# Kernel optimization log

Measured on AMD Instinct MI355X. Metric: run time of the kernel, lower is better.

Reference implementation:

```python
import jax, jax.numpy as jnp
import numpy as np

N_NODES = 50000
N_EDGES = 800000
IN_CH = 128
HID = 128


def setup_inputs() -> dict:
    key = jax.random.key(0)
    ks = jax.random.split(key, 16)
    inp = {
        "x": jax.random.normal(ks[0], (N_NODES, IN_CH), dtype=jnp.float32),
        "edge_index": jax.random.randint(ks[1], (2, N_EDGES), 0, N_NODES, dtype=jnp.int64),
        "batch_size": 1024,
    }
    dims = [(IN_CH, HID), (HID, HID), (HID, HID)]
    for i, (din, dout) in enumerate(dims):
        s = 1.0 / np.sqrt(din)
        inp[f"W_l{i}"] = jax.random.uniform(ks[2 + 4 * i], (dout, din), jnp.float32, -s, s)
        inp[f"b_l{i}"] = jax.random.uniform(ks[3 + 4 * i], (dout,), jnp.float32, -s, s)
        inp[f"W_r{i}"] = jax.random.uniform(ks[4 + 4 * i], (dout, din), jnp.float32, -s, s)
        inp[f"a{i}"] = jnp.full((dout,), 0.25, dtype=jnp.float32)  # PReLU slope
    return inp


def _sage_prelu(x, src, dst, W_l, b_l, W_r, a):
    # mean aggregation of source messages at target nodes
    msg_sum = jax.ops.segment_sum(x[src], dst, num_segments=N_NODES)  # [N, din]
    deg = jax.ops.segment_sum(jnp.ones((src.shape[0],), x.dtype), dst, num_segments=N_NODES)
    agg = msg_sum / jnp.maximum(deg, 1.0)[:, None]
    out = agg @ W_l.T + b_l + x @ W_r.T  # lin_l(aggr) + lin_r(x), bias on lin_l only
    return jnp.where(out > 0, out, a * out)  # per-channel PReLU


def reference(x, edge_index, batch_size, W_l0, b_l0, W_r0, a0, W_l1, b_l1, W_r1, a1, W_l2, b_l2, W_r2, a2):
    src, dst = edge_index[0], edge_index[1]
    x = _sage_prelu(x, src, dst, W_l0, b_l0, W_r0, a0)
    x = _sage_prelu(x, src, dst, W_l1, b_l1, W_r1, a1)
    x = _sage_prelu(x, src, dst, W_l2, b_l2, W_r2, a2)
    return x[:batch_size]
```

## Files before the change

### kernel.cpp

```cpp
#include <hip/hip_runtime.h>

#define NN 50000
#define NE 800000
#define C 128
#define CAP 64
#define DEGS 16
#define EP16 ((NE / 16 + 255) / 256)
#define SPLITB 1563
#define WB 96
#define CB  ((NN + 255) / 256)
#define AGG0B ((NN + 3) / 4)
#define ASTRIDE 136

typedef __attribute__((ext_vector_type(8))) short bf16x8;
typedef __attribute__((ext_vector_type(4))) float f32x4;
typedef unsigned short ushort;

__device__ inline ushort bf16_rn(float f) {
    unsigned u = __builtin_bit_cast(unsigned, f);
    u += 0x7FFF + ((u >> 16) & 1);
    return (ushort)(u >> 16);
}
__device__ inline void split_bf16(float f, ushort& hi, ushort& lo) {
    hi = bf16_rn(f);
    float hif = __builtin_bit_cast(float, (unsigned)hi << 16);
    lo = bf16_rn(f - hif);
}
__device__ inline float bf_lo(unsigned u) { return __builtin_bit_cast(float, u << 16); }
__device__ inline float bf_hi(unsigned u) { return __builtin_bit_cast(float, u & 0xFFFF0000u); }


__global__ __launch_bounds__(256)
void prep_kernel(const int* __restrict__ src, const int* __restrict__ dst,
                 const float* __restrict__ x,
                 const float* __restrict__ W0, const float* __restrict__ W1,
                 const float* __restrict__ W2, const float* __restrict__ W3,
                 const float* __restrict__ W4, const float* __restrict__ W5,
                 int* __restrict__ deg, int* __restrict__ col,
                 ushort* __restrict__ Ah,
                 ushort* __restrict__ Wh, ushort* __restrict__ Wl,
                 int* __restrict__ needed, int rows_out) {
    int t = threadIdx.x;
    if (blockIdx.x < EP16) {
        int e0 = (blockIdx.x * 256 + t) * 16;
        if (e0 < NE) {
            #pragma unroll
            for (int g = 0; g < 4; ++g) {
                int4 d4 = *(const int4*)(dst + e0 + g * 4);
                int4 s4 = *(const int4*)(src + e0 + g * 4);
                int p0 = atomicAdd(&deg[d4.x * DEGS], 1);
                int p1 = atomicAdd(&deg[d4.y * DEGS], 1);
                int p2 = atomicAdd(&deg[d4.z * DEGS], 1);
                int p3 = atomicAdd(&deg[d4.w * DEGS], 1);
                if (p0 < CAP) col[d4.x * CAP + p0] = s4.x;
                if (p1 < CAP) col[d4.y * CAP + p1] = s4.y;
                if (p2 < CAP) col[d4.z * CAP + p2] = s4.z;
                if (p3 < CAP) col[d4.w * CAP + p3] = s4.w;
                if (d4.x < rows_out) needed[s4.x] = 1;
                if (d4.y < rows_out) needed[s4.y] = 1;
                if (d4.z < rows_out) needed[s4.z] = 1;
                if (d4.w < rows_out) needed[s4.w] = 1;
            }
        }
    } else if (blockIdx.x < EP16 + SPLITB) {
        int tid = (blockIdx.x - EP16) * 256 + t;
        const int total = NN * C / 4;
        for (int i = tid; i < total; i += SPLITB * 256) {
            f32x4 v = ((const f32x4*)x)[i];
            ushort h0 = bf16_rn(v.x), h1 = bf16_rn(v.y);
            ushort h2 = bf16_rn(v.z), h3 = bf16_rn(v.w);
            *(uint2*)(Ah + (size_t)i * 4) = make_uint2((unsigned)h0 | ((unsigned)h1 << 16),
                                                       (unsigned)h2 | ((unsigned)h3 << 16));
        }
    } else {
        const float* Ws[6] = {W0, W1, W2, W3, W4, W5};
        int i = (blockIdx.x - EP16 - SPLITB) * 256 + t;
        int mat = i >> 12;
        f32x4 v = ((const f32x4*)Ws[mat])[i & 4095];
        ushort h0, h1, h2, h3, l0, l1, l2, l3;
        split_bf16(v.x, h0, l0);
        split_bf16(v.y, h1, l1);
        split_bf16(v.z, h2, l2);
        split_bf16(v.w, h3, l3);
        *(uint2*)(Wh + (size_t)i * 4) = make_uint2((unsigned)h0 | ((unsigned)h1 << 16),
                                                   (unsigned)h2 | ((unsigned)h3 << 16));
        *(uint2*)(Wl + (size_t)i * 4) = make_uint2((unsigned)l0 | ((unsigned)l1 << 16),
                                                   (unsigned)l2 | ((unsigned)l3 << 16));
    }
}


__global__ __launch_bounds__(256)
void agg_kernel(const ushort* __restrict__ xh, const int* __restrict__ deg,
                const int* __restrict__ col,
                const int* __restrict__ list, const int* __restrict__ countp,
                ushort* __restrict__ aggh, int nodes,
                int aggblocks, const int* __restrict__ needed,
                int* __restrict__ wlist, int* __restrict__ wcnt, int rows_out) {
    if (needed && blockIdx.x >= aggblocks) {
        int i = (blockIdx.x - aggblocks) * 256 + threadIdx.x;
        if (i < NN && (i < rows_out || needed[i])) {
            int p = atomicAdd(wcnt, 1);
            wlist[p] = i;
        }
        return;
    }
    int i = (blockIdx.x * blockDim.x + threadIdx.x) >> 6;
    int lane = threadIdx.x & 63;
    int cnt = list ? *countp : nodes;
    if (i >= cnt) return;
    int node = list ? list[i] : i;
    int quad = lane >> 4;
    int ql   = lane & 15;
    int d = min(deg[node * DEGS], CAP);
    int start = node * CAP;
    int end = start + d;
    const uint4* xr = (const uint4*)xh;
    float a0=0,a1=0,a2=0,a3=0,a4=0,a5=0,a6=0,a7=0;
    int e = start;
    for (; e + 15 < end; e += 16) {
        int i0 = col[e + quad];
        int i1 = col[e + 4 + quad];
        int i2 = col[e + 8 + quad];
        int i3 = col[e + 12 + quad];
        uint4 u0 = xr[(size_t)i0 * 16 + ql];
        uint4 u1 = xr[(size_t)i1 * 16 + ql];
        uint4 u2 = xr[(size_t)i2 * 16 + ql];
        uint4 u3 = xr[(size_t)i3 * 16 + ql];
        a0 += (bf_lo(u0.x) + bf_lo(u1.x)) + (bf_lo(u2.x) + bf_lo(u3.x));
        a1 += (bf_hi(u0.x) + bf_hi(u1.x)) + (bf_hi(u2.x) + bf_hi(u3.x));
        a2 += (bf_lo(u0.y) + bf_lo(u1.y)) + (bf_lo(u2.y) + bf_lo(u3.y));
        a3 += (bf_hi(u0.y) + bf_hi(u1.y)) + (bf_hi(u2.y) + bf_hi(u3.y));
        a4 += (bf_lo(u0.z) + bf_lo(u1.z)) + (bf_lo(u2.z) + bf_lo(u3.z));
        a5 += (bf_hi(u0.z) + bf_hi(u1.z)) + (bf_hi(u2.z) + bf_hi(u3.z));
        a6 += (bf_lo(u0.w) + bf_lo(u1.w)) + (bf_lo(u2.w) + bf_lo(u3.w));
        a7 += (bf_hi(u0.w) + bf_hi(u1.w)) + (bf_hi(u2.w) + bf_hi(u3.w));
    }
    for (; e + 7 < end; e += 8) {
        int i0 = col[e + quad];
        int i1 = col[e + 4 + quad];
        uint4 u0 = xr[(size_t)i0 * 16 + ql];
        uint4 u1 = xr[(size_t)i1 * 16 + ql];
        a0 += bf_lo(u0.x) + bf_lo(u1.x); a1 += bf_hi(u0.x) + bf_hi(u1.x);
        a2 += bf_lo(u0.y) + bf_lo(u1.y); a3 += bf_hi(u0.y) + bf_hi(u1.y);
        a4 += bf_lo(u0.z) + bf_lo(u1.z); a5 += bf_hi(u0.z) + bf_hi(u1.z);
        a6 += bf_lo(u0.w) + bf_lo(u1.w); a7 += bf_hi(u0.w) + bf_hi(u1.w);
    }
    for (; e + 3 < end; e += 4) {
        uint4 u = xr[(size_t)col[e + quad] * 16 + ql];
        a0 += bf_lo(u.x); a1 += bf_hi(u.x);
        a2 += bf_lo(u.y); a3 += bf_hi(u.y);
        a4 += bf_lo(u.z); a5 += bf_hi(u.z);
        a6 += bf_lo(u.w); a7 += bf_hi(u.w);
    }
    int rem = end - e;
    if (quad < rem) {
        uint4 u = xr[(size_t)col[e + quad] * 16 + ql];
        a0 += bf_lo(u.x); a1 += bf_hi(u.x);
        a2 += bf_lo(u.y); a3 += bf_hi(u.y);
        a4 += bf_lo(u.z); a5 += bf_hi(u.z);
        a6 += bf_lo(u.w); a7 += bf_hi(u.w);
    }
    a0 += __shfl_xor(a0, 16, 64); a0 += __shfl_xor(a0, 32, 64);
    a1 += __shfl_xor(a1, 16, 64); a1 += __shfl_xor(a1, 32, 64);
    a2 += __shfl_xor(a2, 16, 64); a2 += __shfl_xor(a2, 32, 64);
    a3 += __shfl_xor(a3, 16, 64); a3 += __shfl_xor(a3, 32, 64);
    a4 += __shfl_xor(a4, 16, 64); a4 += __shfl_xor(a4, 32, 64);
    a5 += __shfl_xor(a5, 16, 64); a5 += __shfl_xor(a5, 32, 64);
    a6 += __shfl_xor(a6, 16, 64); a6 += __shfl_xor(a6, 32, 64);
    a7 += __shfl_xor(a7, 16, 64); a7 += __shfl_xor(a7, 32, 64);
    if (quad == 0) {
        float inv = 1.0f / (float)max(d, 1);
        float m[8] = {a0*inv, a1*inv, a2*inv, a3*inv, a4*inv, a5*inv, a6*inv, a7*inv};
        ushort h[8];
        #pragma unroll
        for (int j = 0; j < 8; ++j) h[j] = bf16_rn(m[j]);
        size_t off = (size_t)node * C + ql * 8;
        *(uint4*)(aggh + off) = make_uint4((unsigned)h[0] | ((unsigned)h[1] << 16),
                                           (unsigned)h[2] | ((unsigned)h[3] << 16),
                                           (unsigned)h[4] | ((unsigned)h[5] << 16),
                                           (unsigned)h[6] | ((unsigned)h[7] << 16));
    }
}


__global__ __launch_bounds__(256, 4)
void gemm_kernel(const ushort* __restrict__ Ag,
                 const ushort* __restrict__ Xh, const ushort* __restrict__ Xl,
                 const float* __restrict__ Xf,
                 const ushort* __restrict__ Wlh, const ushort* __restrict__ Wll,
                 const ushort* __restrict__ Wrh, const ushort* __restrict__ Wrl,
                 const float* __restrict__ bl, const float* __restrict__ slope,
                 const int* __restrict__ list, const int* __restrict__ countp,
                 float* __restrict__ outf, ushort* __restrict__ outh,
                 ushort* __restrict__ outl, int rows) {
    __shared__ ushort Ahi[64 * ASTRIDE];
    __shared__ ushort Alo[64 * ASTRIDE];
    int t = threadIdx.x;
    int lane = t & 63;
    int w = t >> 6;
    int l = lane & 15;
    int q = lane >> 4;
    int row0 = blockIdx.x * 64;
    int cnt = list ? min(*countp, rows) : rows;
    if (row0 >= cnt) return;

    f32x4 acc[4][2];
    #pragma unroll
    for (int mt = 0; mt < 4; ++mt)
        #pragma unroll
        for (int nt = 0; nt < 2; ++nt)
            acc[mt][nt] = (f32x4){0.f, 0.f, 0.f, 0.f};

    #pragma unroll
    for (int mat = 0; mat < 2; ++mat) {
        const ushort* WH = mat ? Wrh : Wlh;
        const ushort* WL = mat ? Wrl : Wll;

        bf16x8 bhi[2][4], blo[2][4];
        #pragma unroll
        for (int nt = 0; nt < 2; ++nt) {
            int n = w * 32 + nt * 16 + l;
            const ushort* wp = WH + (size_t)n * C + q * 8;
            const ushort* wq = WL + (size_t)n * C + q * 8;
            #pragma unroll
            for (int kb = 0; kb < 4; ++kb) {
                bhi[nt][kb] = *(const bf16x8*)(wp + kb * 32);
                blo[nt][kb] = *(const bf16x8*)(wq + kb * 32);
            }
        }

        __syncthreads();
        int ar = t >> 2;
        int aq = t & 3;
        int ridx = min(row0 + ar, cnt - 1);
        int r = list ? list[ridx] : ridx;
        ushort* dh = Ahi + ar * ASTRIDE + aq * 32;
        ushort* dl = Alo + ar * ASTRIDE + aq * 32;
        if (mat == 0) {
            const ushort* ph = Ag + (size_t)r * C + aq * 32;
            #pragma unroll
            for (int i = 0; i < 4; ++i)
                *(uint4*)(dh + i * 8) = *(const uint4*)(ph + i * 8);
        } else if (Xf) {
            const float* px = Xf + (size_t)r * C + aq * 32;
            #pragma unroll
            for (int i = 0; i < 8; ++i) {
                f32x4 v = *(const f32x4*)(px + i * 4);
                ushort h0, h1, h2, h3, l0, l1, l2, l3;
                split_bf16(v.x, h0, l0);
                split_bf16(v.y, h1, l1);
                split_bf16(v.z, h2, l2);
                split_bf16(v.w, h3, l3);
                *(uint2*)(dh + i * 4) = make_uint2((unsigned)h0 | ((unsigned)h1 << 16),
                                                   (unsigned)h2 | ((unsigned)h3 << 16));
                *(uint2*)(dl + i * 4) = make_uint2((unsigned)l0 | ((unsigned)l1 << 16),
                                                   (unsigned)l2 | ((unsigned)l3 << 16));
            }
        } else {
            const ushort* ph = Xh + (size_t)r * C + aq * 32;
            const ushort* pl = Xl + (size_t)r * C + aq * 32;
            #pragma unroll
            for (int i = 0; i < 4; ++i) {
                *(uint4*)(dh + i * 8) = *(const uint4*)(ph + i * 8);
                *(uint4*)(dl + i * 8) = *(const uint4*)(pl + i * 8);
            }
        }
        __syncthreads();

        #pragma unroll
        for (int kb = 0; kb < 4; ++kb) {
            #pragma unroll
            for (int mt = 0; mt < 4; ++mt) {
                int off = (mt * 16 + l) * ASTRIDE + kb * 32 + q * 8;
                bf16x8 ahi = *(const bf16x8*)(Ahi + off);
                #pragma unroll
                for (int nt = 0; nt < 2; ++nt) {
                    acc[mt][nt] = __builtin_amdgcn_mfma_f32_16x16x32_bf16(ahi, bhi[nt][kb], acc[mt][nt], 0, 0, 0);
                    if (mat == 1) {
                        bf16x8 alo = *(const bf16x8*)(Alo + off);
                        acc[mt][nt] = __builtin_amdgcn_mfma_f32_16x16x32_bf16(alo, bhi[nt][kb], acc[mt][nt], 0, 0, 0);
                    }
                    acc[mt][nt] = __builtin_amdgcn_mfma_f32_16x16x32_bf16(ahi, blo[nt][kb], acc[mt][nt], 0, 0, 0);
                }
            }
        }
    }

    #pragma unroll
    for (int nt = 0; nt < 2; ++nt) {
        int n = w * 32 + nt * 16 + l;
        float b = bl[n], s = slope[n];
        #pragma unroll
        for (int mt = 0; mt < 4; ++mt) {
            #pragma unroll
            for (int rg = 0; rg < 4; ++rg) {
                int ridx = row0 + mt * 16 + q * 4 + rg;
                if (ridx < cnt) {
                    int r = list ? list[ridx] : ridx;
                    float v = acc[mt][nt][rg] + b;
                    v = v > 0.f ? v : s * v;
                    if (outf) {
                        outf[(size_t)r * C + n] = v;
                    } else {
                        ushort hh, ll;
                        split_bf16(v, hh, ll);
                        outh[(size_t)r * C + n] = hh;
                        outl[(size_t)r * C + n] = ll;
                    }
                }
            }
        }
    }
}


__global__ __launch_bounds__(256)
void fused_kernel(const ushort* __restrict__ Gsrc,
                  const int* __restrict__ deg, const int* __restrict__ col,
                  const ushort* __restrict__ Xh, const ushort* __restrict__ Xl,
                  const ushort* __restrict__ Wlh, const ushort* __restrict__ Wll,
                  const ushort* __restrict__ Wrh, const ushort* __restrict__ Wrl,
                  const float* __restrict__ bl, const float* __restrict__ slope,
                  float* __restrict__ outf, int rows) {
    __shared__ ushort Ahi[64 * ASTRIDE];
    __shared__ ushort Alo[64 * ASTRIDE];
    int t = threadIdx.x;
    int lane = t & 63;
    int w = t >> 6;
    int l = lane & 15;
    int q = lane >> 4;
    int row0 = blockIdx.x * 64;
    if (row0 >= rows) return;

    f32x4 acc[4][2];
    #pragma unroll
    for (int mt = 0; mt < 4; ++mt)
        #pragma unroll
        for (int nt = 0; nt < 2; ++nt)
            acc[mt][nt] = (f32x4){0.f, 0.f, 0.f, 0.f};

    #pragma unroll
    for (int mat = 0; mat < 2; ++mat) {
        const ushort* WH = mat ? Wrh : Wlh;
        const ushort* WL = mat ? Wrl : Wll;

        bf16x8 bhi[2][4], blo[2][4];
        #pragma unroll
        for (int nt = 0; nt < 2; ++nt) {
            int n = w * 32 + nt * 16 + l;
            const ushort* wp = WH + (size_t)n * C + q * 8;
            const ushort* wq = WL + (size_t)n * C + q * 8;
            #pragma unroll
            for (int kb = 0; kb < 4; ++kb) {
                bhi[nt][kb] = *(const bf16x8*)(wp + kb * 32);
                blo[nt][kb] = *(const bf16x8*)(wq + kb * 32);
            }
        }

        __syncthreads();
        int ar = t >> 2;
        int aq = t & 3;
        int r = min(row0 + ar, rows - 1);
        ushort* dh = Ahi + ar * ASTRIDE + aq * 32;
        ushort* dl = Alo + ar * ASTRIDE + aq * 32;
        if (mat == 0) {
            int d = min(deg[r * DEGS], CAP);
            int base = r * CAP;
            float s[32];
            #pragma unroll
            for (int j = 0; j < 32; ++j) s[j] = 0.f;
#define ACC8(k, u, v) \
            s[(k)+0] += bf_lo((u).x) + bf_lo((v).x); s[(k)+1] += bf_hi((u).x) + bf_hi((v).x); \
            s[(k)+2] += bf_lo((u).y) + bf_lo((v).y); s[(k)+3] += bf_hi((u).y) + bf_hi((v).y); \
            s[(k)+4] += bf_lo((u).z) + bf_lo((v).z); s[(k)+5] += bf_hi((u).z) + bf_hi((v).z); \
            s[(k)+6] += bf_lo((u).w) + bf_lo((v).w); s[(k)+7] += bf_hi((u).w) + bf_hi((v).w);
#define ACC8S(k, u) \
            s[(k)+0] += bf_lo((u).x); s[(k)+1] += bf_hi((u).x); \
            s[(k)+2] += bf_lo((u).y); s[(k)+3] += bf_hi((u).y); \
            s[(k)+4] += bf_lo((u).z); s[(k)+5] += bf_hi((u).z); \
            s[(k)+6] += bf_lo((u).w); s[(k)+7] += bf_hi((u).w);
            int e = 0;
            for (; e + 1 < d; e += 2) {
                int2 c01 = *(const int2*)(col + base + e);
                const uint4* p0 = (const uint4*)Gsrc + (size_t)c01.x * 16 + aq * 4;
                const uint4* p1 = (const uint4*)Gsrc + (size_t)c01.y * 16 + aq * 4;
                uint4 a0 = p0[0], a1 = p0[1], a2 = p0[2], a3 = p0[3];
                uint4 b0 = p1[0], b1 = p1[1], b2 = p1[2], b3 = p1[3];
                ACC8(0, a0, b0) ACC8(8, a1, b1) ACC8(16, a2, b2) ACC8(24, a3, b3)
            }
            if (e < d) {
                int c0 = col[base + e];
                const uint4* p0 = (const uint4*)Gsrc + (size_t)c0 * 16 + aq * 4;
                uint4 a0 = p0[0], a1 = p0[1], a2 = p0[2], a3 = p0[3];
                ACC8S(0, a0) ACC8S(8, a1) ACC8S(16, a2) ACC8S(24, a3)
            }
#undef ACC8
#undef ACC8S
            float inv = 1.0f / (float)max(d, 1);
            #pragma unroll
            for (int i = 0; i < 4; ++i) {
                ushort h[8], o[8];
                #pragma unroll
                for (int j = 0; j < 8; ++j) split_bf16(s[i * 8 + j] * inv, h[j], o[j]);
                *(uint4*)(dh + i * 8) = make_uint4((unsigned)h[0] | ((unsigned)h[1] << 16),
                                                   (unsigned)h[2] | ((unsigned)h[3] << 16),
                                                   (unsigned)h[4] | ((unsigned)h[5] << 16),
                                                   (unsigned)h[6] | ((unsigned)h[7] << 16));
                *(uint4*)(dl + i * 8) = make_uint4((unsigned)o[0] | ((unsigned)o[1] << 16),
                                                   (unsigned)o[2] | ((unsigned)o[3] << 16),
                                                   (unsigned)o[4] | ((unsigned)o[5] << 16),
                                                   (unsigned)o[6] | ((unsigned)o[7] << 16));
            }
        } else {
            const ushort* ph = Xh + (size_t)r * C + aq * 32;
            const ushort* pl = Xl + (size_t)r * C + aq * 32;
            #pragma unroll
            for (int i = 0; i < 4; ++i) {
                *(uint4*)(dh + i * 8) = *(const uint4*)(ph + i * 8);
                *(uint4*)(dl + i * 8) = *(const uint4*)(pl + i * 8);
            }
        }
        __syncthreads();

        #pragma unroll
        for (int kb = 0; kb < 4; ++kb) {
            #pragma unroll
            for (int mt = 0; mt < 4; ++mt) {
                int off = (mt * 16 + l) * ASTRIDE + kb * 32 + q * 8;
                bf16x8 ahi = *(const bf16x8*)(Ahi + off);
                bf16x8 alo = *(const bf16x8*)(Alo + off);
                #pragma unroll
                for (int nt = 0; nt < 2; ++nt) {
                    acc[mt][nt] = __builtin_amdgcn_mfma_f32_16x16x32_bf16(ahi, bhi[nt][kb], acc[mt][nt], 0, 0, 0);
                    acc[mt][nt] = __builtin_amdgcn_mfma_f32_16x16x32_bf16(alo, bhi[nt][kb], acc[mt][nt], 0, 0, 0);
                    acc[mt][nt] = __builtin_amdgcn_mfma_f32_16x16x32_bf16(ahi, blo[nt][kb], acc[mt][nt], 0, 0, 0);
                }
            }
        }
    }

    #pragma unroll
    for (int nt = 0; nt < 2; ++nt) {
        int n = w * 32 + nt * 16 + l;
        float b = bl[n], s = slope[n];
        #pragma unroll
        for (int mt = 0; mt < 4; ++mt) {
            #pragma unroll
            for (int rg = 0; rg < 4; ++rg) {
                int ridx = row0 + mt * 16 + q * 4 + rg;
                if (ridx < rows) {
                    float v = acc[mt][nt][rg] + b;
                    v = v > 0.f ? v : s * v;
                    outf[(size_t)ridx * C + n] = v;
                }
            }
        }
    }
}


extern "C" void kernel_launch(void* const* d_in, const int* in_sizes, int n_in,
                              void* d_out, int out_size, void* d_ws, size_t ws_size,
                              hipStream_t stream) {
    const float* x   = (const float*)d_in[0];
    const int*   src = (const int*)d_in[1];
    const int*   dst = src + NE;
    const float* Wl[3] = {(const float*)d_in[3], (const float*)d_in[7],  (const float*)d_in[11]};
    const float* bl[3] = {(const float*)d_in[4], (const float*)d_in[8],  (const float*)d_in[12]};
    const float* Wr[3] = {(const float*)d_in[5], (const float*)d_in[9],  (const float*)d_in[13]};
    const float* sl[3] = {(const float*)d_in[6], (const float*)d_in[10], (const float*)d_in[14]};

    int*   deg     = (int*)d_ws;
    int*   needed  = deg + NN * DEGS;
    int*   cnt     = needed + 50016;
    int*   col     = cnt + 16;
    int*   list    = col + NN * CAP;
    ushort* Whs    = (ushort*)(list + 50016);
    ushort* Wls    = Whs + 6 * 16384;
    ushort* Gh     = Wls + 6 * 16384;
    ushort* Ah     = Gh + (size_t)NN * C;
    ushort* Al     = Ah + (size_t)NN * C;
    ushort* Bh     = Al + (size_t)NN * C;
    ushort* Bl     = Bh + (size_t)NN * C;

    int rows_out = out_size / C;

    hipMemsetAsync(deg, 0, (NN * DEGS + 50016 + 16) * sizeof(int), stream);

    prep_kernel<<<EP16 + SPLITB + WB, 256, 0, stream>>>(
        src, dst, x, Wl[0], Wr[0], Wl[1], Wr[1], Wl[2], Wr[2],
        deg, col, Ah, Whs, Wls, needed, rows_out);

    agg_kernel<<<AGG0B + CB, 256, 0, stream>>>(Ah, deg, col, nullptr, nullptr, Gh, NN,
                                               AGG0B, needed, list, cnt, rows_out);
    gemm_kernel<<<(NN + 63) / 64, 256, 0, stream>>>(Gh, nullptr, nullptr, x,
                                                    Whs + 0 * 16384, Wls + 0 * 16384,
                                                    Whs + 1 * 16384, Wls + 1 * 16384,
                                                    bl[0], sl[0], nullptr, nullptr,
                                                    nullptr, Bh, Bl, NN);

    agg_kernel<<<AGG0B, 256, 0, stream>>>(Bh, deg, col, list, cnt, Gh, NN,
                                          AGG0B, nullptr, nullptr, nullptr, rows_out);
    gemm_kernel<<<(NN + 63) / 64, 256, 0, stream>>>(Gh, Bh, Bl, nullptr,
                                                    Whs + 2 * 16384, Wls + 2 * 16384,
                                                    Whs + 3 * 16384, Wls + 3 * 16384,
                                                    bl[1], sl[1], list, cnt,
                                                    nullptr, Ah, Al, NN);

    fused_kernel<<<(rows_out + 63) / 64, 256, 0, stream>>>(Ah, deg, col, Ah, Al,
                                                           Whs + 4 * 16384, Wls + 4 * 16384,
                                                           Whs + 5 * 16384, Wls + 5 * 16384,
                                                           bl[2], sl[2],
                                                           (float*)d_out, rows_out);
}
```

Measured before the change: 272.9 us.

## Split per-node degree counters into four sub-buckets and skip unneeded low-part writes

The edge-bucketing atomics now spread each destination node's counter across four padded sub-counters chosen by thread lane, each with its own column bucket of capacity 24. The goal is to reduce atomic contention on hot destination nodes. The aggregation and fused kernels loop over the four buckets and sum their degrees. The GEMM epilogue writes the low bf16 half only for rows that later stages read, which cuts store traffic. The changes cost a larger zero-initialised degree array and more column storage, and a bucket now overflows whenever one lane group gets more than 24 edges for a node.

```diff
diff --git a/kernel.cpp b/kernel.cpp
--- a/kernel.cpp
+++ b/kernel.cpp
@@ -3,8 +3,9 @@
 #define NN 50000
 #define NE 800000
 #define C 128
-#define CAP 64
-#define DEGS 16
+#define BCAP 24
+#define NDEG 64
+#define NCOL 96
 #define EP16 ((NE / 16 + 255) / 256)
 #define SPLITB 1563
 #define WB 96
@@ -43,19 +44,21 @@
     int t = threadIdx.x;
     if (blockIdx.x < EP16) {
         int e0 = (blockIdx.x * 256 + t) * 16;
+        int k16 = (t & 3) * 16;
+        int kb  = (t & 3) * BCAP;
         if (e0 < NE) {
             #pragma unroll
             for (int g = 0; g < 4; ++g) {
                 int4 d4 = *(const int4*)(dst + e0 + g * 4);
                 int4 s4 = *(const int4*)(src + e0 + g * 4);
-                int p0 = atomicAdd(&deg[d4.x * DEGS], 1);
-                int p1 = atomicAdd(&deg[d4.y * DEGS], 1);
-                int p2 = atomicAdd(&deg[d4.z * DEGS], 1);
-                int p3 = atomicAdd(&deg[d4.w * DEGS], 1);
-                if (p0 < CAP) col[d4.x * CAP + p0] = s4.x;
-                if (p1 < CAP) col[d4.y * CAP + p1] = s4.y;
-                if (p2 < CAP) col[d4.z * CAP + p2] = s4.z;
-                if (p3 < CAP) col[d4.w * CAP + p3] = s4.w;
+                int p0 = atomicAdd(&deg[d4.x * NDEG + k16], 1);
+                int p1 = atomicAdd(&deg[d4.y * NDEG + k16], 1);
+                int p2 = atomicAdd(&deg[d4.z * NDEG + k16], 1);
+                int p3 = atomicAdd(&deg[d4.w * NDEG + k16], 1);
+                if (p0 < BCAP) col[d4.x * NCOL + kb + p0] = s4.x;
+                if (p1 < BCAP) col[d4.y * NCOL + kb + p1] = s4.y;
+                if (p2 < BCAP) col[d4.z * NCOL + kb + p2] = s4.z;
+                if (p3 < BCAP) col[d4.w * NCOL + kb + p3] = s4.w;
                 if (d4.x < rows_out) needed[s4.x] = 1;
                 if (d4.y < rows_out) needed[s4.y] = 1;
                 if (d4.z < rows_out) needed[s4.z] = 1;
@@ -90,6 +93,7 @@
 }
 
 
+template<int STAGE>
 __global__ __launch_bounds__(256)
 void agg_kernel(const ushort* __restrict__ xh, const int* __restrict__ deg,
                 const int* __restrict__ col,
@@ -112,55 +116,44 @@
     int node = list ? list[i] : i;
     int quad = lane >> 4;
     int ql   = lane & 15;
-    int d = min(deg[node * DEGS], CAP);
-    int start = node * CAP;
-    int end = start + d;
+    int dk0 = min(deg[node * NDEG +  0], BCAP);
+    int dk1 = min(deg[node * NDEG + 16], BCAP);
+    int dk2 = min(deg[node * NDEG + 32], BCAP);
+    int dk3 = min(deg[node * NDEG + 48], BCAP);
+    int dsum = dk0 + dk1 + dk2 + dk3;
+    int base = node * NCOL;
     const uint4* xr = (const uint4*)xh;
     float a0=0,a1=0,a2=0,a3=0,a4=0,a5=0,a6=0,a7=0;
-    int e = start;
-    for (; e + 15 < end; e += 16) {
-        int i0 = col[e + quad];
-        int i1 = col[e + 4 + quad];
-        int i2 = col[e + 8 + quad];
-        int i3 = col[e + 12 + quad];
-        uint4 u0 = xr[(size_t)i0 * 16 + ql];
-        uint4 u1 = xr[(size_t)i1 * 16 + ql];
-        uint4 u2 = xr[(size_t)i2 * 16 + ql];
-        uint4 u3 = xr[(size_t)i3 * 16 + ql];
-        a0 += (bf_lo(u0.x) + bf_lo(u1.x)) + (bf_lo(u2.x) + bf_lo(u3.x));
-        a1 += (bf_hi(u0.x) + bf_hi(u1.x)) + (bf_hi(u2.x) + bf_hi(u3.x));
-        a2 += (bf_lo(u0.y) + bf_lo(u1.y)) + (bf_lo(u2.y) + bf_lo(u3.y));
-        a3 += (bf_hi(u0.y) + bf_hi(u1.y)) + (bf_hi(u2.y) + bf_hi(u3.y));
-        a4 += (bf_lo(u0.z) + bf_lo(u1.z)) + (bf_lo(u2.z) + bf_lo(u3.z));
-        a5 += (bf_hi(u0.z) + bf_hi(u1.z)) + (bf_hi(u2.z) + bf_hi(u3.z));
-        a6 += (bf_lo(u0.w) + bf_lo(u1.w)) + (bf_lo(u2.w) + bf_lo(u3.w));
-        a7 += (bf_hi(u0.w) + bf_hi(u1.w)) + (bf_hi(u2.w) + bf_hi(u3.w));
-    }
-    for (; e + 7 < end; e += 8) {
-        int i0 = col[e + quad];
-        int i1 = col[e + 4 + quad];
-        uint4 u0 = xr[(size_t)i0 * 16 + ql];
-        uint4 u1 = xr[(size_t)i1 * 16 + ql];
-        a0 += bf_lo(u0.x) + bf_lo(u1.x); a1 += bf_hi(u0.x) + bf_hi(u1.x);
-        a2 += bf_lo(u0.y) + bf_lo(u1.y); a3 += bf_hi(u0.y) + bf_hi(u1.y);
-        a4 += bf_lo(u0.z) + bf_lo(u1.z); a5 += bf_hi(u0.z) + bf_hi(u1.z);
-        a6 += bf_lo(u0.w) + bf_lo(u1.w); a7 += bf_hi(u0.w) + bf_hi(u1.w);
-    }
-    for (; e + 3 < end; e += 4) {
-        uint4 u = xr[(size_t)col[e + quad] * 16 + ql];
-        a0 += bf_lo(u.x); a1 += bf_hi(u.x);
-        a2 += bf_lo(u.y); a3 += bf_hi(u.y);
-        a4 += bf_lo(u.z); a5 += bf_hi(u.z);
-        a6 += bf_lo(u.w); a7 += bf_hi(u.w);
-    }
-    int rem = end - e;
-    if (quad < rem) {
-        uint4 u = xr[(size_t)col[e + quad] * 16 + ql];
-        a0 += bf_lo(u.x); a1 += bf_hi(u.x);
-        a2 += bf_lo(u.y); a3 += bf_hi(u.y);
-        a4 += bf_lo(u.z); a5 += bf_hi(u.z);
-        a6 += bf_lo(u.w); a7 += bf_hi(u.w);
-    }
+#define ACCU(u) \
+    a0 += bf_lo((u).x); a1 += bf_hi((u).x); \
+    a2 += bf_lo((u).y); a3 += bf_hi((u).y); \
+    a4 += bf_lo((u).z); a5 += bf_hi((u).z); \
+    a6 += bf_lo((u).w); a7 += bf_hi((u).w);
+#define BUCKET(bofs, dk) { \
+    int b = base + (bofs); \
+    int e = 0; \
+    for (; e + 7 < (dk); e += 8) { \
+        int i0 = col[b + e + quad]; \
+        int i1 = col[b + e + 4 + quad]; \
+        uint4 u0 = xr[(size_t)i0 * 16 + ql]; \
+        uint4 u1 = xr[(size_t)i1 * 16 + ql]; \
+        ACCU(u0) ACCU(u1) \
+    } \
+    for (; e + 3 < (dk); e += 4) { \
+        uint4 u = xr[(size_t)col[b + e + quad] * 16 + ql]; \
+        ACCU(u) \
+    } \
+    int rem = (dk) - e; \
+    if (quad < rem) { \
+        uint4 u = xr[(size_t)col[b + e + quad] * 16 + ql]; \
+        ACCU(u) \
+    } }
+    BUCKET(0 * BCAP, dk0)
+    BUCKET(1 * BCAP, dk1)
+    BUCKET(2 * BCAP, dk2)
+    BUCKET(3 * BCAP, dk3)
+#undef BUCKET
+#undef ACCU
     a0 += __shfl_xor(a0, 16, 64); a0 += __shfl_xor(a0, 32, 64);
     a1 += __shfl_xor(a1, 16, 64); a1 += __shfl_xor(a1, 32, 64);
     a2 += __shfl_xor(a2, 16, 64); a2 += __shfl_xor(a2, 32, 64);
@@ -170,7 +163,7 @@
     a6 += __shfl_xor(a6, 16, 64); a6 += __shfl_xor(a6, 32, 64);
     a7 += __shfl_xor(a7, 16, 64); a7 += __shfl_xor(a7, 32, 64);
     if (quad == 0) {
-        float inv = 1.0f / (float)max(d, 1);
+        float inv = 1.0f / (float)max(dsum, 1);
         float m[8] = {a0*inv, a1*inv, a2*inv, a3*inv, a4*inv, a5*inv, a6*inv, a7*inv};
         ushort h[8];
         #pragma unroll
@@ -184,6 +177,7 @@
 }
 
 
+template<int LOMODE>
 __global__ __launch_bounds__(256, 4)
 void gemm_kernel(const ushort* __restrict__ Ag,
                  const ushort* __restrict__ Xh, const ushort* __restrict__ Xl,
@@ -192,8 +186,8 @@
                  const ushort* __restrict__ Wrh, const ushort* __restrict__ Wrl,
                  const float* __restrict__ bl, const float* __restrict__ slope,
                  const int* __restrict__ list, const int* __restrict__ countp,
-                 float* __restrict__ outf, ushort* __restrict__ outh,
-                 ushort* __restrict__ outl, int rows) {
+                 ushort* __restrict__ outh, ushort* __restrict__ outl, int rows,
+                 const int* __restrict__ needed, int rows_out) {
     __shared__ ushort Ahi[64 * ASTRIDE];
     __shared__ ushort Alo[64 * ASTRIDE];
     int t = threadIdx.x;
@@ -300,14 +294,12 @@
                     int r = list ? list[ridx] : ridx;
                     float v = acc[mt][nt][rg] + b;
                     v = v > 0.f ? v : s * v;
-                    if (outf) {
-                        outf[(size_t)r * C + n] = v;
-                    } else {
-                        ushort hh, ll;
-                        split_bf16(v, hh, ll);
-                        outh[(size_t)r * C + n] = hh;
-                        outl[(size_t)r * C + n] = ll;
-                    }
+                    ushort hh, ll;
+                    split_bf16(v, hh, ll);
+                    outh[(size_t)r * C + n] = hh;
+                    bool wlo = (LOMODE == 1) ? (r < rows_out || needed[r])
+                                             : (r < rows_out);
+                    if (wlo) outl[(size_t)r * C + n] = ll;
                 }
             }
         }
@@ -365,8 +357,12 @@
         ushort* dh = Ahi + ar * ASTRIDE + aq * 32;
         ushort* dl = Alo + ar * ASTRIDE + aq * 32;
         if (mat == 0) {
-            int d = min(deg[r * DEGS], CAP);
-            int base = r * CAP;
+            int dk0 = min(deg[r * NDEG +  0], BCAP);
+            int dk1 = min(deg[r * NDEG + 16], BCAP);
+            int dk2 = min(deg[r * NDEG + 32], BCAP);
+            int dk3 = min(deg[r * NDEG + 48], BCAP);
+            int dsum = dk0 + dk1 + dk2 + dk3;
+            int base = r * NCOL;
             float s[32];
             #pragma unroll
             for (int j = 0; j < 32; ++j) s[j] = 0.f;
@@ -380,24 +376,31 @@
             s[(k)+2] += bf_lo((u).y); s[(k)+3] += bf_hi((u).y); \
             s[(k)+4] += bf_lo((u).z); s[(k)+5] += bf_hi((u).z); \
             s[(k)+6] += bf_lo((u).w); s[(k)+7] += bf_hi((u).w);
-            int e = 0;
-            for (; e + 1 < d; e += 2) {
-                int2 c01 = *(const int2*)(col + base + e);
-                const uint4* p0 = (const uint4*)Gsrc + (size_t)c01.x * 16 + aq * 4;
-                const uint4* p1 = (const uint4*)Gsrc + (size_t)c01.y * 16 + aq * 4;
-                uint4 a0 = p0[0], a1 = p0[1], a2 = p0[2], a3 = p0[3];
-                uint4 b0 = p1[0], b1 = p1[1], b2 = p1[2], b3 = p1[3];
-                ACC8(0, a0, b0) ACC8(8, a1, b1) ACC8(16, a2, b2) ACC8(24, a3, b3)
-            }
-            if (e < d) {
-                int c0 = col[base + e];
-                const uint4* p0 = (const uint4*)Gsrc + (size_t)c0 * 16 + aq * 4;
-                uint4 a0 = p0[0], a1 = p0[1], a2 = p0[2], a3 = p0[3];
-                ACC8S(0, a0) ACC8S(8, a1) ACC8S(16, a2) ACC8S(24, a3)
-            }
+#define FBUCKET(bofs, dk) { \
+            int b = base + (bofs); \
+            int e = 0; \
+            for (; e + 1 < (dk); e += 2) { \
+                int2 c01 = *(const int2*)(col + b + e); \
+                const uint4* p0 = (const uint4*)Gsrc + (size_t)c01.x * 16 + aq * 4; \
+                const uint4* p1 = (const uint4*)Gsrc + (size_t)c01.y * 16 + aq * 4; \
+                uint4 a0 = p0[0], a1 = p0[1], a2 = p0[2], a3 = p0[3]; \
+                uint4 b0 = p1[0], b1 = p1[1], b2 = p1[2], b3 = p1[3]; \
+                ACC8(0, a0, b0) ACC8(8, a1, b1) ACC8(16, a2, b2) ACC8(24, a3, b3) \
+            } \
+            if (e < (dk)) { \
+                int c0 = col[b + e]; \
+                const uint4* p0 = (const uint4*)Gsrc + (size_t)c0 * 16 + aq * 4; \
+                uint4 a0 = p0[0], a1 = p0[1], a2 = p0[2], a3 = p0[3]; \
+                ACC8S(0, a0) ACC8S(8, a1) ACC8S(16, a2) ACC8S(24, a3) \
+            } }
+            FBUCKET(0 * BCAP, dk0)
+            FBUCKET(1 * BCAP, dk1)
+            FBUCKET(2 * BCAP, dk2)
+            FBUCKET(3 * BCAP, dk3)
+#undef FBUCKET
 #undef ACC8
 #undef ACC8S
-            float inv = 1.0f / (float)max(d, 1);
+            float inv = 1.0f / (float)max(dsum, 1);
             #pragma unroll
             for (int i = 0; i < 4; ++i) {
                 ushort h[8], o[8];
@@ -472,10 +475,10 @@
     const float* sl[3] = {(const float*)d_in[6], (const float*)d_in[10], (const float*)d_in[14]};
 
     int*   deg     = (int*)d_ws;
-    int*   needed  = deg + NN * DEGS;
+    int*   needed  = deg + NN * NDEG;
     int*   cnt     = needed + 50016;
     int*   col     = cnt + 16;
-    int*   list    = col + NN * CAP;
+    int*   list    = col + NN * NCOL;
     ushort* Whs    = (ushort*)(list + 50016);
     ushort* Wls    = Whs + 6 * 16384;
     ushort* Gh     = Wls + 6 * 16384;
@@ -486,27 +489,27 @@
 
     int rows_out = out_size / C;
 
-    hipMemsetAsync(deg, 0, (NN * DEGS + 50016 + 16) * sizeof(int), stream);
+    hipMemsetAsync(deg, 0, (NN * NDEG + 50016 + 16) * sizeof(int), stream);
 
     prep_kernel<<<EP16 + SPLITB + WB, 256, 0, stream>>>(
         src, dst, x, Wl[0], Wr[0], Wl[1], Wr[1], Wl[2], Wr[2],
         deg, col, Ah, Whs, Wls, needed, rows_out);
 
-    agg_kernel<<<AGG0B + CB, 256, 0, stream>>>(Ah, deg, col, nullptr, nullptr, Gh, NN,
-                                               AGG0B, needed, list, cnt, rows_out);
-    gemm_kernel<<<(NN + 63) / 64, 256, 0, stream>>>(Gh, nullptr, nullptr, x,
-                                                    Whs + 0 * 16384, Wls + 0 * 16384,
-                                                    Whs + 1 * 16384, Wls + 1 * 16384,
-                                                    bl[0], sl[0], nullptr, nullptr,
-                                                    nullptr, Bh, Bl, NN);
-
-    agg_kernel<<<AGG0B, 256, 0, stream>>>(Bh, deg, col, list, cnt, Gh, NN,
-                                          AGG0B, nullptr, nullptr, nullptr, rows_out);
-    gemm_kernel<<<(NN + 63) / 64, 256, 0, stream>>>(Gh, Bh, Bl, nullptr,
-                                                    Whs + 2 * 16384, Wls + 2 * 16384,
-                                                    Whs + 3 * 16384, Wls + 3 * 16384,
-                                                    bl[1], sl[1], list, cnt,
-                                                    nullptr, Ah, Al, NN);
+    agg_kernel<0><<<AGG0B + CB, 256, 0, stream>>>(Ah, deg, col, nullptr, nullptr, Gh, NN,
+                                                  AGG0B, needed, list, cnt, rows_out);
+    gemm_kernel<1><<<(NN + 63) / 64, 256, 0, stream>>>(Gh, nullptr, nullptr, x,
+                                                       Whs + 0 * 16384, Wls + 0 * 16384,
+                                                       Whs + 1 * 16384, Wls + 1 * 16384,
+                                                       bl[0], sl[0], nullptr, nullptr,
+                                                       Bh, Bl, NN, needed, rows_out);
+
+    agg_kernel<1><<<AGG0B, 256, 0, stream>>>(Bh, deg, col, list, cnt, Gh, NN,
+                                             AGG0B, nullptr, nullptr, nullptr, rows_out);
+    gemm_kernel<2><<<(NN + 63) / 64, 256, 0, stream>>>(Gh, Bh, Bl, nullptr,
+                                                       Whs + 2 * 16384, Wls + 2 * 16384,
+                                                       Whs + 3 * 16384, Wls + 3 * 16384,
+                                                       bl[1], sl[1], list, cnt,
+                                                       Ah, Al, NN, nullptr, rows_out);
 
     fused_kernel<<<(rows_out + 63) / 64, 256, 0, stream>>>(Ah, deg, col, Ah, Al,
                                                            Whs + 4 * 16384, Wls + 4 * 16384,
```

Measured after the change: 290.7 us. 6.5% more time.

## Store bf16 features in channel-chunked layout and split aggregation by chunk

Applied to the files above, without the earlier changes.

The hi bf16 feature arrays become four 32-channel chunk planes (chunk-major) instead of row-major. The gather kernel now assigns each block to one chunk for four nodes, with each wave spreading its 64 lanes over 16 edges × 4 sub-vectors. The goal is a smaller gather working set per chunk, so chunk-sized node slices stay resident in L2/LLC, and more edge-level parallelism per wave. The cost is four times as many blocks, each reading the column indices again, and more scattered 64-byte reads in place of 256-byte rows.

```diff
diff --git a/kernel.cpp b/kernel.cpp
--- a/kernel.cpp
+++ b/kernel.cpp
@@ -5,11 +5,12 @@
 #define C 128
 #define CAP 64
 #define DEGS 16
+#define CHS (NN * 32)
 #define EP16 ((NE / 16 + 255) / 256)
 #define SPLITB 1563
 #define WB 96
 #define CB  ((NN + 255) / 256)
-#define AGG0B ((NN + 3) / 4)
+#define AGGB NN
 #define ASTRIDE 136
 
 typedef __attribute__((ext_vector_type(8))) short bf16x8;
@@ -69,8 +70,13 @@
             f32x4 v = ((const f32x4*)x)[i];
             ushort h0 = bf16_rn(v.x), h1 = bf16_rn(v.y);
             ushort h2 = bf16_rn(v.z), h3 = bf16_rn(v.w);
-            *(uint2*)(Ah + (size_t)i * 4) = make_uint2((unsigned)h0 | ((unsigned)h1 << 16),
-                                                       (unsigned)h2 | ((unsigned)h3 << 16));
+            int n = i >> 5;
+            int c4 = i & 31;
+            int chunk = c4 >> 3;
+            int off = (c4 & 7) * 4;
+            *(uint2*)(Ah + (size_t)chunk * CHS + (size_t)n * 32 + off) =
+                make_uint2((unsigned)h0 | ((unsigned)h1 << 16),
+                           (unsigned)h2 | ((unsigned)h3 << 16));
         }
     } else {
         const float* Ws[6] = {W0, W1, W2, W3, W4, W5};
@@ -90,6 +96,7 @@
 }
 
 
+template<int STAGE>
 __global__ __launch_bounds__(256)
 void agg_kernel(const ushort* __restrict__ xh, const int* __restrict__ deg,
                 const int* __restrict__ col,
@@ -97,85 +104,54 @@
                 ushort* __restrict__ aggh, int nodes,
                 int aggblocks, const int* __restrict__ needed,
                 int* __restrict__ wlist, int* __restrict__ wcnt, int rows_out) {
-    if (needed && blockIdx.x >= aggblocks) {
-        int i = (blockIdx.x - aggblocks) * 256 + threadIdx.x;
+    if (needed && (int)blockIdx.x >= aggblocks) {
+        int i = ((int)blockIdx.x - aggblocks) * 256 + threadIdx.x;
         if (i < NN && (i < rows_out || needed[i])) {
             int p = atomicAdd(wcnt, 1);
             wlist[p] = i;
         }
         return;
     }
-    int i = (blockIdx.x * blockDim.x + threadIdx.x) >> 6;
+    int wid  = threadIdx.x >> 6;
     int lane = threadIdx.x & 63;
+    int chunk = blockIdx.x & 3;
+    int i = ((blockIdx.x >> 2) << 2) + wid;
     int cnt = list ? *countp : nodes;
     if (i >= cnt) return;
     int node = list ? list[i] : i;
-    int quad = lane >> 4;
-    int ql   = lane & 15;
+    int es  = lane >> 2;
+    int sub = lane & 3;
     int d = min(deg[node * DEGS], CAP);
-    int start = node * CAP;
-    int end = start + d;
-    const uint4* xr = (const uint4*)xh;
+    int base = node * CAP;
+    const uint4* xr = (const uint4*)xh + (size_t)chunk * (NN * 4);
     float a0=0,a1=0,a2=0,a3=0,a4=0,a5=0,a6=0,a7=0;
-    int e = start;
-    for (; e + 15 < end; e += 16) {
-        int i0 = col[e + quad];
-        int i1 = col[e + 4 + quad];
-        int i2 = col[e + 8 + quad];
-        int i3 = col[e + 12 + quad];
-        uint4 u0 = xr[(size_t)i0 * 16 + ql];
-        uint4 u1 = xr[(size_t)i1 * 16 + ql];
-        uint4 u2 = xr[(size_t)i2 * 16 + ql];
-        uint4 u3 = xr[(size_t)i3 * 16 + ql];
-        a0 += (bf_lo(u0.x) + bf_lo(u1.x)) + (bf_lo(u2.x) + bf_lo(u3.x));
-        a1 += (bf_hi(u0.x) + bf_hi(u1.x)) + (bf_hi(u2.x) + bf_hi(u3.x));
-        a2 += (bf_lo(u0.y) + bf_lo(u1.y)) + (bf_lo(u2.y) + bf_lo(u3.y));
-        a3 += (bf_hi(u0.y) + bf_hi(u1.y)) + (bf_hi(u2.y) + bf_hi(u3.y));
-        a4 += (bf_lo(u0.z) + bf_lo(u1.z)) + (bf_lo(u2.z) + bf_lo(u3.z));
-        a5 += (bf_hi(u0.z) + bf_hi(u1.z)) + (bf_hi(u2.z) + bf_hi(u3.z));
-        a6 += (bf_lo(u0.w) + bf_lo(u1.w)) + (bf_lo(u2.w) + bf_lo(u3.w));
-        a7 += (bf_hi(u0.w) + bf_hi(u1.w)) + (bf_hi(u2.w) + bf_hi(u3.w));
-    }
-    for (; e + 7 < end; e += 8) {
-        int i0 = col[e + quad];
-        int i1 = col[e + 4 + quad];
-        uint4 u0 = xr[(size_t)i0 * 16 + ql];
-        uint4 u1 = xr[(size_t)i1 * 16 + ql];
-        a0 += bf_lo(u0.x) + bf_lo(u1.x); a1 += bf_hi(u0.x) + bf_hi(u1.x);
-        a2 += bf_lo(u0.y) + bf_lo(u1.y); a3 += bf_hi(u0.y) + bf_hi(u1.y);
-        a4 += bf_lo(u0.z) + bf_lo(u1.z); a5 += bf_hi(u0.z) + bf_hi(u1.z);
-        a6 += bf_lo(u0.w) + bf_lo(u1.w); a7 += bf_hi(u0.w) + bf_hi(u1.w);
-    }
-    for (; e + 3 < end; e += 4) {
-        uint4 u = xr[(size_t)col[e + quad] * 16 + ql];
+    for (int e = es; e < d; e += 16) {
+        int c = col[base + e];
+        uint4 u = xr[(size_t)c * 4 + sub];
         a0 += bf_lo(u.x); a1 += bf_hi(u.x);
         a2 += bf_lo(u.y); a3 += bf_hi(u.y);
         a4 += bf_lo(u.z); a5 += bf_hi(u.z);
         a6 += bf_lo(u.w); a7 += bf_hi(u.w);
     }
-    int rem = end - e;
-    if (quad < rem) {
-        uint4 u = xr[(size_t)col[e + quad] * 16 + ql];
-        a0 += bf_lo(u.x); a1 += bf_hi(u.x);
-        a2 += bf_lo(u.y); a3 += bf_hi(u.y);
-        a4 += bf_lo(u.z); a5 += bf_hi(u.z);
-        a6 += bf_lo(u.w); a7 += bf_hi(u.w);
-    }
-    a0 += __shfl_xor(a0, 16, 64); a0 += __shfl_xor(a0, 32, 64);
-    a1 += __shfl_xor(a1, 16, 64); a1 += __shfl_xor(a1, 32, 64);
-    a2 += __shfl_xor(a2, 16, 64); a2 += __shfl_xor(a2, 32, 64);
-    a3 += __shfl_xor(a3, 16, 64); a3 += __shfl_xor(a3, 32, 64);
-    a4 += __shfl_xor(a4, 16, 64); a4 += __shfl_xor(a4, 32, 64);
-    a5 += __shfl_xor(a5, 16, 64); a5 += __shfl_xor(a5, 32, 64);
-    a6 += __shfl_xor(a6, 16, 64); a6 += __shfl_xor(a6, 32, 64);
-    a7 += __shfl_xor(a7, 16, 64); a7 += __shfl_xor(a7, 32, 64);
-    if (quad == 0) {
+    #pragma unroll
+    for (int ofs = 4; ofs < 64; ofs <<= 1) {
+        a0 += __shfl_xor(a0, ofs, 64);
+        a1 += __shfl_xor(a1, ofs, 64);
+        a2 += __shfl_xor(a2, ofs, 64);
+        a3 += __shfl_xor(a3, ofs, 64);
+        a4 += __shfl_xor(a4, ofs, 64);
+        a5 += __shfl_xor(a5, ofs, 64);
+        a6 += __shfl_xor(a6, ofs, 64);
+        a7 += __shfl_xor(a7, ofs, 64);
+    }
+    if (lane < 4) {
         float inv = 1.0f / (float)max(d, 1);
-        float m[8] = {a0*inv, a1*inv, a2*inv, a3*inv, a4*inv, a5*inv, a6*inv, a7*inv};
         ushort h[8];
-        #pragma unroll
-        for (int j = 0; j < 8; ++j) h[j] = bf16_rn(m[j]);
-        size_t off = (size_t)node * C + ql * 8;
+        h[0] = bf16_rn(a0 * inv); h[1] = bf16_rn(a1 * inv);
+        h[2] = bf16_rn(a2 * inv); h[3] = bf16_rn(a3 * inv);
+        h[4] = bf16_rn(a4 * inv); h[5] = bf16_rn(a5 * inv);
+        h[6] = bf16_rn(a6 * inv); h[7] = bf16_rn(a7 * inv);
+        size_t off = (size_t)node * C + chunk * 32 + lane * 8;
         *(uint4*)(aggh + off) = make_uint4((unsigned)h[0] | ((unsigned)h[1] << 16),
                                            (unsigned)h[2] | ((unsigned)h[3] << 16),
                                            (unsigned)h[4] | ((unsigned)h[5] << 16),
@@ -184,6 +160,7 @@
 }
 
 
+template<int STAGE>
 __global__ __launch_bounds__(256, 4)
 void gemm_kernel(const ushort* __restrict__ Ag,
                  const ushort* __restrict__ Xh, const ushort* __restrict__ Xl,
@@ -192,8 +169,7 @@
                  const ushort* __restrict__ Wrh, const ushort* __restrict__ Wrl,
                  const float* __restrict__ bl, const float* __restrict__ slope,
                  const int* __restrict__ list, const int* __restrict__ countp,
-                 float* __restrict__ outf, ushort* __restrict__ outh,
-                 ushort* __restrict__ outl, int rows) {
+                 ushort* __restrict__ outh, ushort* __restrict__ outl, int rows) {
     __shared__ ushort Ahi[64 * ASTRIDE];
     __shared__ ushort Alo[64 * ASTRIDE];
     int t = threadIdx.x;
@@ -258,7 +234,7 @@
                                                    (unsigned)l2 | ((unsigned)l3 << 16));
             }
         } else {
-            const ushort* ph = Xh + (size_t)r * C + aq * 32;
+            const ushort* ph = Xh + (size_t)aq * CHS + (size_t)r * 32;
             const ushort* pl = Xl + (size_t)r * C + aq * 32;
             #pragma unroll
             for (int i = 0; i < 4; ++i) {
@@ -300,14 +276,10 @@
                     int r = list ? list[ridx] : ridx;
                     float v = acc[mt][nt][rg] + b;
                     v = v > 0.f ? v : s * v;
-                    if (outf) {
-                        outf[(size_t)r * C + n] = v;
-                    } else {
-                        ushort hh, ll;
-                        split_bf16(v, hh, ll);
-                        outh[(size_t)r * C + n] = hh;
-                        outl[(size_t)r * C + n] = ll;
-                    }
+                    ushort hh, ll;
+                    split_bf16(v, hh, ll);
+                    outh[(size_t)w * CHS + (size_t)r * 32 + nt * 16 + l] = hh;
+                    outl[(size_t)r * C + n] = ll;
                 }
             }
         }
@@ -367,6 +339,7 @@
         if (mat == 0) {
             int d = min(deg[r * DEGS], CAP);
             int base = r * CAP;
+            const uint4* xr = (const uint4*)Gsrc + (size_t)aq * (NN * 4);
             float s[32];
             #pragma unroll
             for (int j = 0; j < 32; ++j) s[j] = 0.f;
@@ -383,15 +356,15 @@
             int e = 0;
             for (; e + 1 < d; e += 2) {
                 int2 c01 = *(const int2*)(col + base + e);
-                const uint4* p0 = (const uint4*)Gsrc + (size_t)c01.x * 16 + aq * 4;
-                const uint4* p1 = (const uint4*)Gsrc + (size_t)c01.y * 16 + aq * 4;
+                const uint4* p0 = xr + (size_t)c01.x * 4;
+                const uint4* p1 = xr + (size_t)c01.y * 4;
                 uint4 a0 = p0[0], a1 = p0[1], a2 = p0[2], a3 = p0[3];
                 uint4 b0 = p1[0], b1 = p1[1], b2 = p1[2], b3 = p1[3];
                 ACC8(0, a0, b0) ACC8(8, a1, b1) ACC8(16, a2, b2) ACC8(24, a3, b3)
             }
             if (e < d) {
                 int c0 = col[base + e];
-                const uint4* p0 = (const uint4*)Gsrc + (size_t)c0 * 16 + aq * 4;
+                const uint4* p0 = xr + (size_t)c0 * 4;
                 uint4 a0 = p0[0], a1 = p0[1], a2 = p0[2], a3 = p0[3];
                 ACC8S(0, a0) ACC8S(8, a1) ACC8S(16, a2) ACC8S(24, a3)
             }
@@ -413,7 +386,7 @@
                                                    (unsigned)o[6] | ((unsigned)o[7] << 16));
             }
         } else {
-            const ushort* ph = Xh + (size_t)r * C + aq * 32;
+            const ushort* ph = Xh + (size_t)aq * CHS + (size_t)r * 32;
             const ushort* pl = Xl + (size_t)r * C + aq * 32;
             #pragma unroll
             for (int i = 0; i < 4; ++i) {
@@ -492,21 +465,21 @@
         src, dst, x, Wl[0], Wr[0], Wl[1], Wr[1], Wl[2], Wr[2],
         deg, col, Ah, Whs, Wls, needed, rows_out);
 
-    agg_kernel<<<AGG0B + CB, 256, 0, stream>>>(Ah, deg, col, nullptr, nullptr, Gh, NN,
-                                               AGG0B, needed, list, cnt, rows_out);
-    gemm_kernel<<<(NN + 63) / 64, 256, 0, stream>>>(Gh, nullptr, nullptr, x,
-                                                    Whs + 0 * 16384, Wls + 0 * 16384,
-                                                    Whs + 1 * 16384, Wls + 1 * 16384,
-                                                    bl[0], sl[0], nullptr, nullptr,
-                                                    nullptr, Bh, Bl, NN);
-
-    agg_kernel<<<AGG0B, 256, 0, stream>>>(Bh, deg, col, list, cnt, Gh, NN,
-                                          AGG0B, nullptr, nullptr, nullptr, rows_out);
-    gemm_kernel<<<(NN + 63) / 64, 256, 0, stream>>>(Gh, Bh, Bl, nullptr,
-                                                    Whs + 2 * 16384, Wls + 2 * 16384,
-                                                    Whs + 3 * 16384, Wls + 3 * 16384,
-                                                    bl[1], sl[1], list, cnt,
-                                                    nullptr, Ah, Al, NN);
+    agg_kernel<0><<<AGGB + CB, 256, 0, stream>>>(Ah, deg, col, nullptr, nullptr, Gh, NN,
+                                                 AGGB, needed, list, cnt, rows_out);
+    gemm_kernel<0><<<(NN + 63) / 64, 256, 0, stream>>>(Gh, nullptr, nullptr, x,
+                                                       Whs + 0 * 16384, Wls + 0 * 16384,
+                                                       Whs + 1 * 16384, Wls + 1 * 16384,
+                                                       bl[0], sl[0], nullptr, nullptr,
+                                                       Bh, Bl, NN);
+
+    agg_kernel<1><<<AGGB, 256, 0, stream>>>(Bh, deg, col, list, cnt, Gh, NN,
+                                            AGGB, nullptr, nullptr, nullptr, rows_out);
+    gemm_kernel<1><<<(NN + 63) / 64, 256, 0, stream>>>(Gh, Bh, Bl, nullptr,
+                                                       Whs + 2 * 16384, Wls + 2 * 16384,
+                                                       Whs + 3 * 16384, Wls + 3 * 16384,
+                                                       bl[1], sl[1], list, cnt,
+                                                       Ah, Al, NN);
 
     fused_kernel<<<(rows_out + 63) / 64, 256, 0, stream>>>(Ah, deg, col, Ah, Al,
                                                            Whs + 4 * 16384, Wls + 4 * 16384,
```

Measured after the change: 332.4 us. +21.8%, slower.
